# Kernel tuning notes

Measured on AMD Instinct MI355X. Metric: run time of the kernel, lower is better.

Reference implementation:

```python
import jax, jax.numpy as jnp
import numpy as np

E = 8           # ensemble size
D_IN = 512      # input_dim (state+action)
H = 1024        # hidden size, arch=[1024, 1024]
D_OUT = 1       # output_dim (Q value)
LN_EPS = 1e-5


def setup_inputs() -> dict:
    key = jax.random.key(0)
    ks = jax.random.split(key, 8)
    s1 = 1.0 / np.sqrt(D_IN)
    s2 = 1.0 / np.sqrt(H)
    return {
        "x": jax.random.normal(ks[0], (16384, D_IN), dtype=jnp.float32),
        # stacked per-ensemble parameters: leading axis E
        "W1": jax.random.uniform(ks[1], (E, D_IN, H), jnp.float32, -s1, s1),
        "b1": jax.random.uniform(ks[2], (E, H), jnp.float32, -s1, s1),
        "g1": jnp.ones((E, H), jnp.float32),
        "be1": jnp.zeros((E, H), jnp.float32),
        "W2": jax.random.uniform(ks[3], (E, H, H), jnp.float32, -s2, s2),
        "b2": jax.random.uniform(ks[4], (E, H), jnp.float32, -s2, s2),
        "g2": jnp.ones((E, H), jnp.float32),
        "be2": jnp.zeros((E, H), jnp.float32),
        "W3": jax.random.uniform(ks[5], (E, H, D_OUT), jnp.float32, -s2, s2),
        "b3": jax.random.uniform(ks[6], (E, D_OUT), jnp.float32, -s2, s2),
    }


def _layer_norm(h, g, b):
    # h: [E, B, H]; g, b: [E, H] -> broadcast over batch
    mu = jnp.mean(h, axis=-1, keepdims=True)
    var = jnp.mean(jnp.square(h - mu), axis=-1, keepdims=True)
    return (h - mu) * jax.lax.rsqrt(var + LN_EPS) * g[:, None, :] + b[:, None, :]


def reference(x, W1, b1, g1, be1, W2, b2, g2, be2, W3, b3):
    # Layer 1: all ensemble members as one batched GEMM on shared input
    h = jnp.einsum('bd,edh->ebh', x, W1) + b1[:, None, :]       # [E, B, H]
    h = jax.nn.relu(_layer_norm(h, g1, be1))
    # Layer 2
    h = jnp.einsum('ebd,edh->ebh', h, W2) + b2[:, None, :]      # [E, B, H]
    h = jax.nn.relu(_layer_norm(h, g2, be2))
    # Head (identity head activation)
    qs = jnp.einsum('ebd,edo->ebo', h, W3) + b3[:, None, :]      # [E, B, 1]
    q = jnp.min(qs, axis=0)                                      # [B, 1]
    return (q, qs)
```

## Files before the change

### kernel.cpp

```cpp
#include <hip/hip_runtime.h>
#include <hip/hip_bf16.h>
#include <stdint.h>

#define EN    8
#define DIN   512
#define HID   1024
#define BATCH 16384
#define LN_EPS 1e-5f

typedef __bf16   bf16x8 __attribute__((ext_vector_type(8)));
typedef float    f32x4  __attribute__((ext_vector_type(4)));
typedef uint16_t u16x8  __attribute__((ext_vector_type(8)));
typedef uint16_t u16x4  __attribute__((ext_vector_type(4)));
typedef float    fl4    __attribute__((ext_vector_type(4)));

__device__ __forceinline__ uint16_t f2bf(float f) {
  uint32_t x = __builtin_bit_cast(uint32_t, f);
  uint32_t r = (x + 0x7fffu + ((x >> 16) & 1u)) >> 16;
  return (uint16_t)r;
}
__device__ __forceinline__ float bf2f(uint16_t u) {
  return __builtin_bit_cast(float, (uint32_t)u << 16);
}

__device__ __forceinline__ void gload16(const uint16_t* g, uint16_t* lds) {
  __builtin_amdgcn_global_load_lds(
      (const __attribute__((address_space(1))) uint32_t*)g,
      (__attribute__((address_space(3))) uint32_t*)lds, 16, 0, 0);
}

__device__ __forceinline__ f32x4 MF(bf16x8 a, bf16x8 b, f32x4 c) {
  return __builtin_amdgcn_mfma_f32_16x16x32_bf16(a, b, c, 0, 0, 0);
}

__global__ __launch_bounds__(256) void cvt_bf16(const float* __restrict__ src,
                                                uint16_t* __restrict__ dst, long n) {
  long i = ((long)blockIdx.x * 256 + threadIdx.x) * 4;
  if (i >= n) return;
  fl4 v = *(const fl4*)(src + i);
  u16x4 o;
  #pragma unroll
  for (int j = 0; j < 4; ++j) o[j] = f2bf(v[j]);
  *(u16x4*)(dst + i) = o;
}

__global__ __launch_bounds__(256) void transpose_cvt(const float* __restrict__ src,
                                                     uint16_t* __restrict__ dst,
                                                     int R, int C) {
  __shared__ float tile[32][33];
  const int e = blockIdx.z;
  const int c0 = blockIdx.x * 32;
  const int r0 = blockIdx.y * 32;
  const int tx = threadIdx.x & 31, ty = threadIdx.x >> 5;
  const float* s = src + (size_t)e * R * C;
  uint16_t*    d = dst + (size_t)e * R * C;
  #pragma unroll
  for (int i = 0; i < 32; i += 8)
    tile[ty + i][tx] = s[(size_t)(r0 + ty + i) * C + (c0 + tx)];
  __syncthreads();
  #pragma unroll
  for (int i = 0; i < 32; i += 8)
    d[(size_t)(c0 + ty + i) * R + (r0 + tx)] = f2bf(tile[tx][ty + i]);
}

__global__ __launch_bounds__(512, 2) void gemm256(
    const uint16_t* __restrict__ A, size_t a_estride,
    const uint16_t* __restrict__ Bt,
    const float*    __restrict__ bias,
    uint16_t*       __restrict__ C,
    int M, int K) {
  __shared__ __attribute__((aligned(16))) char lds[131072];
  const int tid = threadIdx.x;
  const int bx  = blockIdx.x;
  const int e   = bx & 7;
  const int t   = bx >> 3;
  const int mt  = t >> 2;
  const int nt  = t & 3;
  const int NT  = K >> 6;
  const int HT  = NT * 4;

  const uint16_t* Ae = A + (size_t)e * a_estride + (size_t)(mt * 256) * K;
  const uint16_t* Be = Bt + ((size_t)e * HID + nt * 256) * K;

  const int l  = tid & 63, wid = tid >> 6;
  const int wr = wid >> 2, wc = wid & 3;
  const int fr = l & 15, kq = l >> 4, f7 = fr & 7;

  const int srow = tid >> 3;
  const int k8s  = (tid & 7) ^ (srow & 7);
  const uint16_t* pA = Ae + (size_t)srow * K + k8s * 8;
  const uint16_t* pB = Be + (size_t)srow * K + k8s * 8;
  char* ldst = lds + tid * 16;

  const int aoff = wr * 16384 + fr * 128 + ((kq ^ f7) << 4);
  const int boff = 32768 + (wc >> 1) * 16384 + (((wc & 1) * 64 + fr) << 7) + ((kq ^ f7) << 4);

  f32x4 acc[8][4];
  #pragma unroll
  for (int i = 0; i < 8; ++i)
    #pragma unroll
    for (int j = 0; j < 4; ++j) acc[i][j] = (f32x4)0.0f;

  auto STAGE = [&](int ht) {
    const int kt2 = ht >> 2, wh = ht & 3;
    char* db = ldst + (kt2 & 1) * 65536;
    if (wh >= 2) {
      const int h = wh - 2;
      const uint16_t* sp = pA + (size_t)(h * 128) * K + kt2 * 64;
      char* d = db + h * 16384;
      gload16(sp, (uint16_t*)d);
      gload16(sp + (size_t)64 * K, (uint16_t*)(d + 8192));
    } else {
      const uint16_t* sp = pB + (size_t)(wh * 128) * K + kt2 * 64;
      char* d = db + 32768 + wh * 16384;
      gload16(sp, (uint16_t*)d);
      gload16(sp + (size_t)64 * K, (uint16_t*)(d + 8192));
    }
  };

  int s = 0;
  for (; s < 7; ++s) STAGE(s);
  asm volatile("s_waitcnt vmcnt(6)" ::: "memory");
  asm volatile("s_barrier" ::: "memory");

  for (int kt = 0; kt < NT; ++kt) {
    const char* rb = lds + (kt & 1) * 65536;
    bf16x8 af[4][2], bv[4][2];
    #pragma unroll
    for (int mi = 0; mi < 4; ++mi) {
      af[mi][0] = *(const bf16x8*)(rb + (aoff + mi * 2048));
      af[mi][1] = *(const bf16x8*)(rb + ((aoff + mi * 2048) ^ 64));
    }
    #pragma unroll
    for (int ni = 0; ni < 4; ++ni) {
      bv[ni][0] = *(const bf16x8*)(rb + (boff + ni * 2048));
      bv[ni][1] = *(const bf16x8*)(rb + ((boff + ni * 2048) ^ 64));
    }
    if (s < HT) STAGE(s++);
    asm volatile("s_barrier" ::: "memory");
    asm volatile("s_waitcnt lgkmcnt(0)" ::: "memory");
    __builtin_amdgcn_s_setprio(1);
    #pragma unroll
    for (int mi = 0; mi < 4; ++mi)
      #pragma unroll
      for (int ni = 0; ni < 2; ++ni) {
        acc[mi][ni] = MF(af[mi][0], bv[ni][0], acc[mi][ni]);
        acc[mi][ni] = MF(af[mi][1], bv[ni][1], acc[mi][ni]);
      }
    __builtin_amdgcn_s_setprio(0);
    asm volatile("s_barrier" ::: "memory");
    if (s < HT) STAGE(s++);
    asm volatile("s_barrier" ::: "memory");
    __builtin_amdgcn_s_setprio(1);
    #pragma unroll
    for (int mi = 0; mi < 4; ++mi)
      #pragma unroll
      for (int ni = 2; ni < 4; ++ni) {
        acc[mi][ni] = MF(af[mi][0], bv[ni][0], acc[mi][ni]);
        acc[mi][ni] = MF(af[mi][1], bv[ni][1], acc[mi][ni]);
      }
    __builtin_amdgcn_s_setprio(0);
    asm volatile("s_barrier" ::: "memory");
    #pragma unroll
    for (int mi = 0; mi < 4; ++mi) {
      af[mi][0] = *(const bf16x8*)(rb + (aoff + (mi + 4) * 2048));
      af[mi][1] = *(const bf16x8*)(rb + ((aoff + (mi + 4) * 2048) ^ 64));
    }
    if (s < HT) STAGE(s++);
    asm volatile("s_barrier" ::: "memory");
    asm volatile("s_waitcnt lgkmcnt(0)" ::: "memory");
    __builtin_amdgcn_s_setprio(1);
    #pragma unroll
    for (int mi = 0; mi < 4; ++mi)
      #pragma unroll
      for (int ni = 0; ni < 2; ++ni) {
        acc[mi + 4][ni] = MF(af[mi][0], bv[ni][0], acc[mi + 4][ni]);
        acc[mi + 4][ni] = MF(af[mi][1], bv[ni][1], acc[mi + 4][ni]);
      }
    __builtin_amdgcn_s_setprio(0);
    asm volatile("s_barrier" ::: "memory");
    if (s < HT) STAGE(s++);
    if (kt < NT - 2)       asm volatile("s_waitcnt vmcnt(6)" ::: "memory");
    else if (kt == NT - 2) asm volatile("s_waitcnt vmcnt(0)" ::: "memory");
    asm volatile("s_barrier" ::: "memory");
    __builtin_amdgcn_s_setprio(1);
    #pragma unroll
    for (int mi = 0; mi < 4; ++mi)
      #pragma unroll
      for (int ni = 2; ni < 4; ++ni) {
        acc[mi + 4][ni] = MF(af[mi][0], bv[ni][0], acc[mi + 4][ni]);
        acc[mi + 4][ni] = MF(af[mi][1], bv[ni][1], acc[mi + 4][ni]);
      }
    __builtin_amdgcn_s_setprio(0);
    asm volatile("s_barrier" ::: "memory");
  }

  const int col0 = nt * 256 + wc * 64 + fr;
  const int row0 = mt * 256 + wr * 128 + kq * 4;
  float bvv[4];
  #pragma unroll
  for (int ni = 0; ni < 4; ++ni) bvv[ni] = bias[(size_t)e * HID + col0 + ni * 16];
  #pragma unroll
  for (int mi = 0; mi < 8; ++mi) {
    #pragma unroll
    for (int i = 0; i < 4; ++i) {
      const int rg = row0 + mi * 16 + i;
      uint16_t* cp = C + ((size_t)e * M + rg) * HID + col0;
      #pragma unroll
      for (int ni = 0; ni < 4; ++ni)
        cp[ni * 16] = f2bf(acc[mi][ni][i] + bvv[ni]);
    }
  }
}

__global__ __launch_bounds__(256) void ln_relu(uint16_t* __restrict__ h,
                                               const float* __restrict__ g,
                                               const float* __restrict__ be,
                                               int kshift) {
  const int wid = threadIdx.x >> 6, l = threadIdx.x & 63;
  const long row = (long)blockIdx.x * 4 + wid;
  const int e = (int)(row >> kshift);
  uint16_t* p = h + row * HID;

  u16x8 s0 = *(const u16x8*)(p + l * 8);
  u16x8 s1 = *(const u16x8*)(p + 512 + l * 8);
  float v[16];
  #pragma unroll
  for (int j = 0; j < 8; ++j) { v[j] = bf2f(s0[j]); v[8 + j] = bf2f(s1[j]); }

  float sum = 0.f, sq = 0.f;
  #pragma unroll
  for (int j = 0; j < 16; ++j) { sum += v[j]; sq += v[j] * v[j]; }
  #pragma unroll
  for (int m = 1; m < 64; m <<= 1) {
    sum += __shfl_xor(sum, m);
    sq  += __shfl_xor(sq, m);
  }
  const float mu  = sum * (1.0f / HID);
  const float var = sq * (1.0f / HID) - mu * mu;
  const float rs  = rsqrtf(var + LN_EPS);

  const float* gp = g  + (size_t)e * HID;
  const float* bp = be + (size_t)e * HID;
  u16x8 o0, o1;
  #pragma unroll
  for (int j = 0; j < 8; ++j) {
    const int c0 = l * 8 + j, c1 = 512 + l * 8 + j;
    float x0 = (v[j]     - mu) * rs * gp[c0] + bp[c0];
    float x1 = (v[8 + j] - mu) * rs * gp[c1] + bp[c1];
    o0[j] = f2bf(fmaxf(x0, 0.f));
    o1[j] = f2bf(fmaxf(x1, 0.f));
  }
  *(u16x8*)(p + l * 8) = o0;
  *(u16x8*)(p + 512 + l * 8) = o1;
}

__global__ __launch_bounds__(256) void ln_head(const uint16_t* __restrict__ h,
                                               const float* __restrict__ g,
                                               const float* __restrict__ be,
                                               const float* __restrict__ W3,
                                               const float* __restrict__ b3,
                                               float* __restrict__ out,
                                               int b0, int CB) {
  __shared__ float qsh[EN];
  const int wv = threadIdx.x >> 6, l = threadIdx.x & 63;
  const long b = blockIdx.x;
  #pragma unroll
  for (int ee = 0; ee < 2; ++ee) {
    const int e = wv + ee * 4;
    const uint16_t* p = h + ((size_t)e * CB + b) * HID;
    u16x8 s0 = *(const u16x8*)(p + l * 8);
    u16x8 s1 = *(const u16x8*)(p + 512 + l * 8);
    float v[16];
    #pragma unroll
    for (int j = 0; j < 8; ++j) { v[j] = bf2f(s0[j]); v[8 + j] = bf2f(s1[j]); }
    float sum = 0.f, sq = 0.f;
    #pragma unroll
    for (int j = 0; j < 16; ++j) { sum += v[j]; sq += v[j] * v[j]; }
    #pragma unroll
    for (int m = 1; m < 64; m <<= 1) {
      sum += __shfl_xor(sum, m);
      sq  += __shfl_xor(sq, m);
    }
    const float mu  = sum * (1.0f / HID);
    const float var = sq * (1.0f / HID) - mu * mu;
    const float rs  = rsqrtf(var + LN_EPS);
    const float* gp = g  + (size_t)e * HID;
    const float* bp = be + (size_t)e * HID;
    const float* w  = W3 + (size_t)e * HID;
    float dot = 0.f;
    #pragma unroll
    for (int j = 0; j < 8; ++j) {
      const int c0 = l * 8 + j, c1 = 512 + l * 8 + j;
      float x0 = fmaxf((v[j]     - mu) * rs * gp[c0] + bp[c0], 0.f);
      float x1 = fmaxf((v[8 + j] - mu) * rs * gp[c1] + bp[c1], 0.f);
      dot += x0 * w[c0] + x1 * w[c1];
    }
    #pragma unroll
    for (int m = 1; m < 64; m <<= 1) dot += __shfl_xor(dot, m);
    if (l == 0) {
      const float qe = dot + b3[e];
      qsh[e] = qe;
      out[BATCH + (size_t)e * BATCH + b0 + b] = qe;
    }
  }
  __syncthreads();
  if (threadIdx.x == 0) {
    float m = qsh[0];
    #pragma unroll
    for (int i = 1; i < EN; ++i) m = fminf(m, qsh[i]);
    out[b0 + b] = m;
  }
}

extern "C" void kernel_launch(void* const* d_in, const int* in_sizes, int n_in,
                              void* d_out, int out_size, void* d_ws, size_t ws_size,
                              hipStream_t stream) {
  const float* x   = (const float*)d_in[0];
  const float* W1  = (const float*)d_in[1];
  const float* b1  = (const float*)d_in[2];
  const float* g1  = (const float*)d_in[3];
  const float* be1 = (const float*)d_in[4];
  const float* W2  = (const float*)d_in[5];
  const float* b2  = (const float*)d_in[6];
  const float* g2  = (const float*)d_in[7];
  const float* be2 = (const float*)d_in[8];
  const float* W3  = (const float*)d_in[9];
  const float* b3  = (const float*)d_in[10];
  float* out = (float*)d_out;

  char* ws = (char*)d_ws;
  uint16_t* xb  = (uint16_t*)ws; ws += (size_t)BATCH * DIN * 2;
  uint16_t* w1t = (uint16_t*)ws; ws += (size_t)EN * DIN * HID * 2;
  uint16_t* w2t = (uint16_t*)ws; ws += (size_t)EN * HID * HID * 2;
  size_t fixed = (size_t)(ws - (char*)d_ws);

  size_t avail = (ws_size > fixed) ? (ws_size - fixed) : 0;
  const size_t per_row = 2ULL * EN * HID * 2ULL;
  int CB = BATCH;
  while (CB > 256 && (size_t)CB * per_row > avail) CB >>= 1;
  const int nchunks = BATCH / CB;
  const int kshift = __builtin_ctz(CB);

  uint16_t* h1 = (uint16_t*)ws; ws += (size_t)EN * CB * HID * 2;
  uint16_t* h2 = (uint16_t*)ws;

  cvt_bf16<<<(BATCH * DIN / 4 + 255) / 256, 256, 0, stream>>>(x, xb, (long)BATCH * DIN);
  transpose_cvt<<<dim3(HID / 32, DIN / 32, EN), 256, 0, stream>>>(W1, w1t, DIN, HID);
  transpose_cvt<<<dim3(HID / 32, HID / 32, EN), 256, 0, stream>>>(W2, w2t, HID, HID);

  const int gblocks = (CB / 256) * (HID / 256) * EN;

  for (int c = 0; c < nchunks; ++c) {
    const int b0 = c * CB;
    gemm256<<<gblocks, 512, 0, stream>>>(xb + (size_t)b0 * DIN, (size_t)0,
                                         w1t, b1, h1, CB, DIN);
    ln_relu<<<(EN * CB) / 4, 256, 0, stream>>>(h1, g1, be1, kshift);
    gemm256<<<gblocks, 512, 0, stream>>>(h1, (size_t)CB * HID,
                                         w2t, b2, h2, CB, HID);
    ln_head<<<CB, 256, 0, stream>>>(h2, g2, be2, W3, b3, out, b0, CB);
  }
}
```

Before: 683.9 us.

## Stage GEMM epilogue through LDS for coalesced bf16 stores; reorder pipeline waits

The GEMM epilogue used to write scattered 2-byte bf16 values straight to global memory. It now adds the bias, writes the accumulators to LDS with a swizzled layout, and reads them back so each thread emits two 16-byte vector stores of contiguous row data. The main loop also drops explicit lgkmcnt waits, moves a barrier to after the A-fragment reloads, and moves the vmcnt wait to after the last MFMA block so global loads overlap more of the compute. The LDS staging costs extra syncs per row block, and removing the lgkmcnt waits relies on the compiler inserting the needed dependency waits.

New measurement: 710.2 us. 3.8% more time.

```diff
diff --git a/kernel.cpp b/kernel.cpp
--- a/kernel.cpp
+++ b/kernel.cpp
@@ -138,7 +138,6 @@
     }
     if (s < HT) STAGE(s++);
     asm volatile("s_barrier" ::: "memory");
-    asm volatile("s_waitcnt lgkmcnt(0)" ::: "memory");
     __builtin_amdgcn_s_setprio(1);
     #pragma unroll
     for (int mi = 0; mi < 4; ++mi)
@@ -160,15 +159,14 @@
         acc[mi][ni] = MF(af[mi][1], bv[ni][1], acc[mi][ni]);
       }
     __builtin_amdgcn_s_setprio(0);
-    asm volatile("s_barrier" ::: "memory");
     #pragma unroll
     for (int mi = 0; mi < 4; ++mi) {
       af[mi][0] = *(const bf16x8*)(rb + (aoff + (mi + 4) * 2048));
       af[mi][1] = *(const bf16x8*)(rb + ((aoff + (mi + 4) * 2048) ^ 64));
     }
+    asm volatile("s_barrier" ::: "memory");
     if (s < HT) STAGE(s++);
     asm volatile("s_barrier" ::: "memory");
-    asm volatile("s_waitcnt lgkmcnt(0)" ::: "memory");
     __builtin_amdgcn_s_setprio(1);
     #pragma unroll
     for (int mi = 0; mi < 4; ++mi)
@@ -180,8 +178,6 @@
     __builtin_amdgcn_s_setprio(0);
     asm volatile("s_barrier" ::: "memory");
     if (s < HT) STAGE(s++);
-    if (kt < NT - 2)       asm volatile("s_waitcnt vmcnt(6)" ::: "memory");
-    else if (kt == NT - 2) asm volatile("s_waitcnt vmcnt(0)" ::: "memory");
     asm volatile("s_barrier" ::: "memory");
     __builtin_amdgcn_s_setprio(1);
     #pragma unroll
@@ -192,24 +188,44 @@
         acc[mi + 4][ni] = MF(af[mi][1], bv[ni][1], acc[mi + 4][ni]);
       }
     __builtin_amdgcn_s_setprio(0);
+    if (kt < NT - 2)       asm volatile("s_waitcnt vmcnt(6)" ::: "memory");
+    else if (kt == NT - 2) asm volatile("s_waitcnt vmcnt(0)" ::: "memory");
     asm volatile("s_barrier" ::: "memory");
   }
 
   const int col0 = nt * 256 + wc * 64 + fr;
-  const int row0 = mt * 256 + wr * 128 + kq * 4;
   float bvv[4];
   #pragma unroll
   for (int ni = 0; ni < 4; ++ni) bvv[ni] = bias[(size_t)e * HID + col0 + ni * 16];
+
+  float* lsl = (float*)lds;
+  const int rs = tid >> 8;
+  const int rr = (tid >> 4) & 15;
+  const int rc = (tid & 15) * 16;
   #pragma unroll
   for (int mi = 0; mi < 8; ++mi) {
-    #pragma unroll
-    for (int i = 0; i < 4; ++i) {
-      const int rg = row0 + mi * 16 + i;
-      uint16_t* cp = C + ((size_t)e * M + rg) * HID + col0;
-      #pragma unroll
-      for (int ni = 0; ni < 4; ++ni)
-        cp[ni * 16] = f2bf(acc[mi][ni][i] + bvv[ni]);
-    }
+    __syncthreads();
+    #pragma unroll
+    for (int ni = 0; ni < 4; ++ni) {
+      const int c = wc * 64 + ni * 16 + fr;
+      f32x4 v = acc[mi][ni];
+      #pragma unroll
+      for (int i = 0; i < 4; ++i) v[i] += bvv[ni];
+      const int fi = wr * 5120 + c * 20 + ((kq * 4) ^ ((((c >> 4) & 3)) << 2));
+      *(f32x4*)(lsl + fi) = v;
+    }
+    __syncthreads();
+    const int rgl = mt * 256 + rs * 128 + mi * 16 + rr;
+    uint16_t* cp = C + ((size_t)e * M + rgl) * HID + nt * 256 + rc;
+    u16x8 o0, o1;
+    #pragma unroll
+    for (int j = 0; j < 8; ++j) {
+      const int c0 = rc + j, c1 = rc + 8 + j;
+      o0[j] = f2bf(lsl[rs * 5120 + c0 * 20 + (rr ^ ((((c0 >> 4) & 3)) << 2))]);
+      o1[j] = f2bf(lsl[rs * 5120 + c1 * 20 + (rr ^ ((((c1 >> 4) & 3)) << 2))]);
+    }
+    *(u16x8*)cp = o0;
+    *(u16x8*)(cp + 8) = o1;
   }
 }
 
```

## Replace 256x256 GEMM tile with 256x128 BK=32 triple-buffered pipeline

Applied to the files above, without the earlier changes.

The bf16 MFMA GEMM moves from a 256x256 output tile with BK=64 double buffering to a 256x128 tile with BK=32 and a three-stage LDS ring. The inner loop drops to one barrier per K step, the LDS swizzle is rebuilt for 64-byte rows, and launch bounds now ask for 4 blocks per CU. The goal is higher occupancy and less barrier overhead so load latency hides better. The cost is lower arithmetic intensity per tile: each A tile is loaded twice as often from global memory, and smaller K steps mean more loop iterations.

Measured after the change: 677.5 us. No clear change (-0.9%).

```diff
diff --git a/kernel.cpp b/kernel.cpp
--- a/kernel.cpp
+++ b/kernel.cpp
@@ -7,6 +7,10 @@
 #define HID   1024
 #define BATCH 16384
 #define LN_EPS 1e-5f
+
+#define BM 256
+#define BN 128
+#define BK 32
 
 typedef __bf16   bf16x8 __attribute__((ext_vector_type(8)));
 typedef float    f32x4  __attribute__((ext_vector_type(4)));
@@ -63,145 +67,84 @@
     d[(size_t)(c0 + ty + i) * R + (r0 + tx)] = f2bf(tile[tx][ty + i]);
 }
 
-__global__ __launch_bounds__(512, 2) void gemm256(
+__global__ __launch_bounds__(512, 4) void gemm_rb(
     const uint16_t* __restrict__ A, size_t a_estride,
     const uint16_t* __restrict__ Bt,
     const float*    __restrict__ bias,
     uint16_t*       __restrict__ C,
     int M, int K) {
-  __shared__ __attribute__((aligned(16))) char lds[131072];
+  __shared__ __attribute__((aligned(16))) char lds[73728];
   const int tid = threadIdx.x;
   const int bx  = blockIdx.x;
   const int e   = bx & 7;
   const int t   = bx >> 3;
-  const int mt  = t >> 2;
-  const int nt  = t & 3;
-  const int NT  = K >> 6;
-  const int HT  = NT * 4;
-
-  const uint16_t* Ae = A + (size_t)e * a_estride + (size_t)(mt * 256) * K;
-  const uint16_t* Be = Bt + ((size_t)e * HID + nt * 256) * K;
+  const int mt  = t >> 3;
+  const int nt  = t & 7;
+  const int NT  = K >> 5;
+
+  const uint16_t* Ae = A + (size_t)e * a_estride + (size_t)(mt * BM) * K;
+  const uint16_t* Be = Bt + ((size_t)e * HID + nt * BN) * K;
 
   const int l  = tid & 63, wid = tid >> 6;
-  const int wr = wid >> 2, wc = wid & 3;
-  const int fr = l & 15, kq = l >> 4, f7 = fr & 7;
-
-  const int srow = tid >> 3;
-  const int k8s  = (tid & 7) ^ (srow & 7);
-  const uint16_t* pA = Ae + (size_t)srow * K + k8s * 8;
-  const uint16_t* pB = Be + (size_t)srow * K + k8s * 8;
-  char* ldst = lds + tid * 16;
-
-  const int aoff = wr * 16384 + fr * 128 + ((kq ^ f7) << 4);
-  const int boff = 32768 + (wc >> 1) * 16384 + (((wc & 1) * 64 + fr) << 7) + ((kq ^ f7) << 4);
-
-  f32x4 acc[8][4];
-  #pragma unroll
-  for (int i = 0; i < 8; ++i)
+  const int wr = wid >> 1, wc = wid & 1;
+  const int fr = l & 15, kq = l >> 4;
+  const int swf = (fr ^ (fr >> 2)) & 3;
+
+  const int srow  = tid >> 2;
+  const int sunit = (tid & 3) ^ ((srow ^ (srow >> 2)) & 3);
+  const uint16_t* pA = Ae + (size_t)srow * K + sunit * 8;
+  const uint16_t* pB = Be + (size_t)srow * K + sunit * 8;
+  char* const ld_t = lds + tid * 16;
+
+  const int aoff = (wr * 64 + fr) * 64 + ((kq ^ swf) << 4);
+  const int boff = 16384 + (wc * 64 + fr) * 64 + ((kq ^ swf) << 4);
+
+  f32x4 acc[4][4];
+  #pragma unroll
+  for (int i = 0; i < 4; ++i)
     #pragma unroll
     for (int j = 0; j < 4; ++j) acc[i][j] = (f32x4)0.0f;
 
-  auto STAGE = [&](int ht) {
-    const int kt2 = ht >> 2, wh = ht & 3;
-    char* db = ldst + (kt2 & 1) * 65536;
-    if (wh >= 2) {
-      const int h = wh - 2;
-      const uint16_t* sp = pA + (size_t)(h * 128) * K + kt2 * 64;
-      char* d = db + h * 16384;
-      gload16(sp, (uint16_t*)d);
-      gload16(sp + (size_t)64 * K, (uint16_t*)(d + 8192));
-    } else {
-      const uint16_t* sp = pB + (size_t)(wh * 128) * K + kt2 * 64;
-      char* d = db + 32768 + wh * 16384;
-      gload16(sp, (uint16_t*)d);
-      gload16(sp + (size_t)64 * K, (uint16_t*)(d + 8192));
-    }
+  auto STAGE = [&](int kt) {
+    char* db = ld_t + (kt % 3) * 24576;
+    const uint16_t* a0 = pA + kt * BK;
+    gload16(a0, (uint16_t*)db);
+    gload16(a0 + (size_t)128 * K, (uint16_t*)(db + 8192));
+    gload16(pB + kt * BK, (uint16_t*)(db + 16384));
   };
 
-  int s = 0;
-  for (; s < 7; ++s) STAGE(s);
-  asm volatile("s_waitcnt vmcnt(6)" ::: "memory");
-  asm volatile("s_barrier" ::: "memory");
+  STAGE(0);
+  STAGE(1);
+  asm volatile("s_waitcnt vmcnt(3)" ::: "memory");
+  __builtin_amdgcn_s_barrier();
 
   for (int kt = 0; kt < NT; ++kt) {
-    const char* rb = lds + (kt & 1) * 65536;
-    bf16x8 af[4][2], bv[4][2];
-    #pragma unroll
-    for (int mi = 0; mi < 4; ++mi) {
-      af[mi][0] = *(const bf16x8*)(rb + (aoff + mi * 2048));
-      af[mi][1] = *(const bf16x8*)(rb + ((aoff + mi * 2048) ^ 64));
-    }
-    #pragma unroll
-    for (int ni = 0; ni < 4; ++ni) {
-      bv[ni][0] = *(const bf16x8*)(rb + (boff + ni * 2048));
-      bv[ni][1] = *(const bf16x8*)(rb + ((boff + ni * 2048) ^ 64));
-    }
-    if (s < HT) STAGE(s++);
-    asm volatile("s_barrier" ::: "memory");
-    asm volatile("s_waitcnt lgkmcnt(0)" ::: "memory");
+    if (kt + 2 < NT) STAGE(kt + 2);
+    const char* rb = lds + (kt % 3) * 24576;
+    bf16x8 af[4], bv[4];
+    #pragma unroll
+    for (int mi = 0; mi < 4; ++mi) af[mi] = *(const bf16x8*)(rb + aoff + mi * 1024);
+    #pragma unroll
+    for (int ni = 0; ni < 4; ++ni) bv[ni] = *(const bf16x8*)(rb + boff + ni * 1024);
     __builtin_amdgcn_s_setprio(1);
     #pragma unroll
-    for (int mi = 0; mi < 4; ++mi)
+    for (int ni = 0; ni < 4; ++ni)
       #pragma unroll
-      for (int ni = 0; ni < 2; ++ni) {
-        acc[mi][ni] = MF(af[mi][0], bv[ni][0], acc[mi][ni]);
-        acc[mi][ni] = MF(af[mi][1], bv[ni][1], acc[mi][ni]);
-      }
+      for (int mi = 0; mi < 4; ++mi)
+        acc[mi][ni] = MF(af[mi], bv[ni], acc[mi][ni]);
     __builtin_amdgcn_s_setprio(0);
-    asm volatile("s_barrier" ::: "memory");
-    if (s < HT) STAGE(s++);
-    asm volatile("s_barrier" ::: "memory");
-    __builtin_amdgcn_s_setprio(1);
-    #pragma unroll
-    for (int mi = 0; mi < 4; ++mi)
-      #pragma unroll
-      for (int ni = 2; ni < 4; ++ni) {
-        acc[mi][ni] = MF(af[mi][0], bv[ni][0], acc[mi][ni]);
-        acc[mi][ni] = MF(af[mi][1], bv[ni][1], acc[mi][ni]);
-      }
-    __builtin_amdgcn_s_setprio(0);
-    asm volatile("s_barrier" ::: "memory");
-    #pragma unroll
-    for (int mi = 0; mi < 4; ++mi) {
-      af[mi][0] = *(const bf16x8*)(rb + (aoff + (mi + 4) * 2048));
-      af[mi][1] = *(const bf16x8*)(rb + ((aoff + (mi + 4) * 2048) ^ 64));
-    }
-    if (s < HT) STAGE(s++);
-    asm volatile("s_barrier" ::: "memory");
-    asm volatile("s_waitcnt lgkmcnt(0)" ::: "memory");
-    __builtin_amdgcn_s_setprio(1);
-    #pragma unroll
-    for (int mi = 0; mi < 4; ++mi)
-      #pragma unroll
-      for (int ni = 0; ni < 2; ++ni) {
-        acc[mi + 4][ni] = MF(af[mi][0], bv[ni][0], acc[mi + 4][ni]);
-        acc[mi + 4][ni] = MF(af[mi][1], bv[ni][1], acc[mi + 4][ni]);
-      }
-    __builtin_amdgcn_s_setprio(0);
-    asm volatile("s_barrier" ::: "memory");
-    if (s < HT) STAGE(s++);
-    if (kt < NT - 2)       asm volatile("s_waitcnt vmcnt(6)" ::: "memory");
-    else if (kt == NT - 2) asm volatile("s_waitcnt vmcnt(0)" ::: "memory");
-    asm volatile("s_barrier" ::: "memory");
-    __builtin_amdgcn_s_setprio(1);
-    #pragma unroll
-    for (int mi = 0; mi < 4; ++mi)
-      #pragma unroll
-      for (int ni = 2; ni < 4; ++ni) {
-        acc[mi + 4][ni] = MF(af[mi][0], bv[ni][0], acc[mi + 4][ni]);
-        acc[mi + 4][ni] = MF(af[mi][1], bv[ni][1], acc[mi + 4][ni]);
-      }
-    __builtin_amdgcn_s_setprio(0);
-    asm volatile("s_barrier" ::: "memory");
-  }
-
-  const int col0 = nt * 256 + wc * 64 + fr;
-  const int row0 = mt * 256 + wr * 128 + kq * 4;
+    if (kt + 2 < NT)      asm volatile("s_waitcnt vmcnt(3)" ::: "memory");
+    else if (kt + 1 < NT) asm volatile("s_waitcnt vmcnt(0)" ::: "memory");
+    if (kt + 1 < NT) __builtin_amdgcn_s_barrier();
+  }
+
+  const int col0 = nt * BN + wc * 64 + fr;
+  const int row0 = mt * BM + wr * 64 + kq * 4;
   float bvv[4];
   #pragma unroll
   for (int ni = 0; ni < 4; ++ni) bvv[ni] = bias[(size_t)e * HID + col0 + ni * 16];
   #pragma unroll
-  for (int mi = 0; mi < 8; ++mi) {
+  for (int mi = 0; mi < 4; ++mi) {
     #pragma unroll
     for (int i = 0; i < 4; ++i) {
       const int rg = row0 + mi * 16 + i;
@@ -349,14 +292,14 @@
   transpose_cvt<<<dim3(HID / 32, DIN / 32, EN), 256, 0, stream>>>(W1, w1t, DIN, HID);
   transpose_cvt<<<dim3(HID / 32, HID / 32, EN), 256, 0, stream>>>(W2, w2t, HID, HID);
 
-  const int gblocks = (CB / 256) * (HID / 256) * EN;
+  const int gblocks = (CB / BM) * (HID / BN) * EN;
 
   for (int c = 0; c < nchunks; ++c) {
     const int b0 = c * CB;
-    gemm256<<<gblocks, 512, 0, stream>>>(xb + (size_t)b0 * DIN, (size_t)0,
+    gemm_rb<<<gblocks, 512, 0, stream>>>(xb + (size_t)b0 * DIN, (size_t)0,
                                          w1t, b1, h1, CB, DIN);
     ln_relu<<<(EN * CB) / 4, 256, 0, stream>>>(h1, g1, be1, kshift);
-    gemm256<<<gblocks, 512, 0, stream>>>(h1, (size_t)CB * HID,
+    gemm_rb<<<gblocks, 512, 0, stream>>>(h1, (size_t)CB * HID,
                                          w2t, b2, h2, CB, HID);
     ln_head<<<CB, 256, 0, stream>>>(h2, g2, be2, W3, b3, out, b0, CB);
   }
```

## Reorder LDS tile layout and interleave B fragment loads with MFMA phases

Applied to the files above, without the earlier changes.

Restructures the LDS layout so A and B halves interleave across four 16KB quadrants, and reorders which global-to-LDS stage loads land in which quadrant. B fragment reads are split so the second half is loaded just before it is needed, and the explicit lgkmcnt(0) waits are removed. The vmcnt wait moves after the last MFMA block so global loads overlap more compute. The aim is more overlap between LDS reads, async global loads and MFMA. The risk is a race or wrong ordering, since the compiler must now insert the LDS waits itself.

Measured after the change: 683.2 us. About the same (-0.1%).

```diff
diff --git a/kernel.cpp b/kernel.cpp
--- a/kernel.cpp
+++ b/kernel.cpp
@@ -23,10 +23,10 @@
   return __builtin_bit_cast(float, (uint32_t)u << 16);
 }
 
-__device__ __forceinline__ void gload16(const uint16_t* g, uint16_t* lds) {
+__device__ __forceinline__ void gload16(const uint16_t* g, char* lds_d) {
   __builtin_amdgcn_global_load_lds(
       (const __attribute__((address_space(1))) uint32_t*)g,
-      (__attribute__((address_space(3))) uint32_t*)lds, 16, 0, 0);
+      (__attribute__((address_space(3))) uint32_t*)lds_d, 16, 0, 0);
 }
 
 __device__ __forceinline__ f32x4 MF(bf16x8 a, bf16x8 b, f32x4 c) {
@@ -87,13 +87,13 @@
   const int fr = l & 15, kq = l >> 4, f7 = fr & 7;
 
   const int srow = tid >> 3;
-  const int k8s  = (tid & 7) ^ (srow & 7);
-  const uint16_t* pA = Ae + (size_t)srow * K + k8s * 8;
-  const uint16_t* pB = Be + (size_t)srow * K + k8s * 8;
-  char* ldst = lds + tid * 16;
-
-  const int aoff = wr * 16384 + fr * 128 + ((kq ^ f7) << 4);
-  const int boff = 32768 + (wc >> 1) * 16384 + (((wc & 1) * 64 + fr) << 7) + ((kq ^ f7) << 4);
+  const int su   = (tid & 7) ^ (srow & 7);
+  const uint16_t* sA0 = Ae + (size_t)srow * K + su * 8;
+  const uint16_t* sB0 = Be + (size_t)srow * K + su * 8;
+  char* const dst0 = lds + tid * 16;
+
+  const int rdA = wr * 8192 + fr * 128 + ((kq ^ f7) << 4);
+  const int rdB = ((wc < 2) ? 16384 : 32768) + (wc & 1) * 8192 + fr * 128 + ((kq ^ f7) << 4);
 
   f32x4 acc[8][4];
   #pragma unroll
@@ -101,44 +101,42 @@
     #pragma unroll
     for (int j = 0; j < 4; ++j) acc[i][j] = (f32x4)0.0f;
 
-  auto STAGE = [&](int ht) {
-    const int kt2 = ht >> 2, wh = ht & 3;
-    char* db = ldst + (kt2 & 1) * 65536;
-    if (wh >= 2) {
-      const int h = wh - 2;
-      const uint16_t* sp = pA + (size_t)(h * 128) * K + kt2 * 64;
-      char* d = db + h * 16384;
-      gload16(sp, (uint16_t*)d);
-      gload16(sp + (size_t)64 * K, (uint16_t*)(d + 8192));
-    } else {
-      const uint16_t* sp = pB + (size_t)(wh * 128) * K + kt2 * 64;
-      char* d = db + 32768 + wh * 16384;
-      gload16(sp, (uint16_t*)d);
-      gload16(sp + (size_t)64 * K, (uint16_t*)(d + 8192));
+  auto STAGE = [&](int H) {
+    const int tH = H >> 2, w = H & 3;
+    char* dst = dst0 + ((tH & 1) << 16) + (w << 14);
+    const size_t ko = (size_t)tH << 6;
+    switch (w) {
+      case 0: gload16(sA0 + ko, dst);
+              gload16(sA0 + (size_t)128 * K + ko, dst + 8192); break;
+      case 1: gload16(sB0 + ko, dst);
+              gload16(sB0 + (size_t)64 * K + ko, dst + 8192); break;
+      case 2: gload16(sB0 + (size_t)128 * K + ko, dst);
+              gload16(sB0 + (size_t)192 * K + ko, dst + 8192); break;
+      default: gload16(sA0 + (size_t)64 * K + ko, dst);
+               gload16(sA0 + (size_t)192 * K + ko, dst + 8192); break;
     }
   };
 
-  int s = 0;
-  for (; s < 7; ++s) STAGE(s);
+  int H = 0;
+  for (; H < 7; ++H) STAGE(H);
   asm volatile("s_waitcnt vmcnt(6)" ::: "memory");
   asm volatile("s_barrier" ::: "memory");
 
+  bf16x8 af[4][2], bv[4][2];
   for (int kt = 0; kt < NT; ++kt) {
-    const char* rb = lds + (kt & 1) * 65536;
-    bf16x8 af[4][2], bv[4][2];
+    const char* rb = lds + ((kt & 1) << 16);
     #pragma unroll
     for (int mi = 0; mi < 4; ++mi) {
-      af[mi][0] = *(const bf16x8*)(rb + (aoff + mi * 2048));
-      af[mi][1] = *(const bf16x8*)(rb + ((aoff + mi * 2048) ^ 64));
-    }
-    #pragma unroll
-    for (int ni = 0; ni < 4; ++ni) {
-      bv[ni][0] = *(const bf16x8*)(rb + (boff + ni * 2048));
-      bv[ni][1] = *(const bf16x8*)(rb + ((boff + ni * 2048) ^ 64));
-    }
-    if (s < HT) STAGE(s++);
-    asm volatile("s_barrier" ::: "memory");
-    asm volatile("s_waitcnt lgkmcnt(0)" ::: "memory");
+      af[mi][0] = *(const bf16x8*)(rb + (rdA + mi * 2048));
+      af[mi][1] = *(const bf16x8*)(rb + ((rdA + mi * 2048) ^ 64));
+    }
+    #pragma unroll
+    for (int ni = 0; ni < 2; ++ni) {
+      bv[ni][0] = *(const bf16x8*)(rb + (rdB + ni * 2048));
+      bv[ni][1] = *(const bf16x8*)(rb + ((rdB + ni * 2048) ^ 64));
+    }
+    if (H < HT) STAGE(H++);
+    asm volatile("s_barrier" ::: "memory");
     __builtin_amdgcn_s_setprio(1);
     #pragma unroll
     for (int mi = 0; mi < 4; ++mi)
@@ -149,7 +147,12 @@
       }
     __builtin_amdgcn_s_setprio(0);
     asm volatile("s_barrier" ::: "memory");
-    if (s < HT) STAGE(s++);
+    #pragma unroll
+    for (int ni = 2; ni < 4; ++ni) {
+      bv[ni][0] = *(const bf16x8*)(rb + (rdB + ni * 2048));
+      bv[ni][1] = *(const bf16x8*)(rb + ((rdB + ni * 2048) ^ 64));
+    }
+    if (H < HT) STAGE(H++);
     asm volatile("s_barrier" ::: "memory");
     __builtin_amdgcn_s_setprio(1);
     #pragma unroll
@@ -163,12 +166,11 @@
     asm volatile("s_barrier" ::: "memory");
     #pragma unroll
     for (int mi = 0; mi < 4; ++mi) {
-      af[mi][0] = *(const bf16x8*)(rb + (aoff + (mi + 4) * 2048));
-      af[mi][1] = *(const bf16x8*)(rb + ((aoff + (mi + 4) * 2048) ^ 64));
-    }
-    if (s < HT) STAGE(s++);
-    asm volatile("s_barrier" ::: "memory");
-    asm volatile("s_waitcnt lgkmcnt(0)" ::: "memory");
+      af[mi][0] = *(const bf16x8*)(rb + (rdA + 49152 + mi * 2048));
+      af[mi][1] = *(const bf16x8*)(rb + ((rdA + 49152 + mi * 2048) ^ 64));
+    }
+    if (H < HT) STAGE(H++);
+    asm volatile("s_barrier" ::: "memory");
     __builtin_amdgcn_s_setprio(1);
     #pragma unroll
     for (int mi = 0; mi < 4; ++mi)
@@ -179,9 +181,7 @@
       }
     __builtin_amdgcn_s_setprio(0);
     asm volatile("s_barrier" ::: "memory");
-    if (s < HT) STAGE(s++);
-    if (kt < NT - 2)       asm volatile("s_waitcnt vmcnt(6)" ::: "memory");
-    else if (kt == NT - 2) asm volatile("s_waitcnt vmcnt(0)" ::: "memory");
+    if (H < HT) STAGE(H++);
     asm volatile("s_barrier" ::: "memory");
     __builtin_amdgcn_s_setprio(1);
     #pragma unroll
@@ -192,6 +192,8 @@
         acc[mi + 4][ni] = MF(af[mi][1], bv[ni][1], acc[mi + 4][ni]);
       }
     __builtin_amdgcn_s_setprio(0);
+    if (kt < NT - 2)       asm volatile("s_waitcnt vmcnt(6)" ::: "memory");
+    else if (kt == NT - 2) asm volatile("s_waitcnt vmcnt(0)" ::: "memory");
     asm volatile("s_barrier" ::: "memory");
   }
 
```
